# Kernel tuning notes

Hardware: AMD Instinct MI355X
Metric: run time of the kernel (lower is better)

## Reference

```python
import jax, jax.numpy as jnp
import numpy as np
from jax import lax

IMAGE_SIZE = 512
MIN_LEVEL, MAX_LEVEL = 3, 7
NUM_SCALES = 3
RATIOS = (1.0, 0.5, 2.0)
BASE_SCALE = 4
PRE_NMS = 5000
POST_NMS = 100
IOU_THR = 0.5
SCORE_THR = 0.2
NUM_CLASSES = 90
BATCH = 8


def _anchors():
    """Multiscale anchors [N,4] in (y1,x1,y2,x2) pixel coords, N=49104 for 512."""
    all_boxes = []
    for level in range(MIN_LEVEL, MAX_LEVEL + 1):
        stride = 2 ** level
        feat = IMAGE_SIZE // stride
        cy = (np.arange(feat, dtype=np.float32) + 0.5) * stride
        cx = (np.arange(feat, dtype=np.float32) + 0.5) * stride
        yv, xv = np.meshgrid(cy, cx, indexing='ij')
        yv = yv.reshape(-1)
        xv = xv.reshape(-1)
        half = []  # (half_h, half_w) per anchor config, 9 per cell
        for i in range(NUM_SCALES):
            base = (2.0 ** (i / 3.0)) * stride * BASE_SCALE
            for r in RATIOS:
                half.append((base / np.sqrt(r) / 2.0, base * np.sqrt(r) / 2.0))
        half = np.asarray(half, dtype=np.float32)  # [9,2]
        boxes = np.stack([
            yv[:, None] - half[None, :, 0],
            xv[:, None] - half[None, :, 1],
            yv[:, None] + half[None, :, 0],
            xv[:, None] + half[None, :, 1],
        ], axis=-1)  # [feat*feat, 9, 4]
        all_boxes.append(boxes.reshape(-1, 4))
    return np.concatenate(all_boxes, axis=0).astype(np.float32)


def setup_inputs() -> dict:
    key = jax.random.key(0)
    k1, k2 = jax.random.split(key)
    n = 49104
    box_deltas = jax.random.normal(k1, (BATCH, n, 4), jnp.float32) * 0.1
    cls_logits = jax.random.normal(k2, (BATCH, n, NUM_CLASSES), jnp.float32)
    return {"box_deltas": box_deltas, "cls_logits": cls_logits}


def _decode(anchors, deltas):
    # Delta2Box with mean=None/std=None: standard (dy,dx,dh,dw) decode.
    ah = anchors[:, 2] - anchors[:, 0]
    aw = anchors[:, 3] - anchors[:, 1]
    acy = (anchors[:, 0] + anchors[:, 2]) * 0.5
    acx = (anchors[:, 1] + anchors[:, 3]) * 0.5
    dy, dx, dh, dw = deltas[..., 0], deltas[..., 1], deltas[..., 2], deltas[..., 3]
    cy = dy * ah + acy
    cx = dx * aw + acx
    h = jnp.exp(dh) * ah
    w = jnp.exp(dw) * aw
    return jnp.stack([cy - h * 0.5, cx - w * 0.5, cy + h * 0.5, cx + w * 0.5], axis=-1)


def _iou_one_many(box, boxes):
    yy1 = jnp.maximum(box[0], boxes[:, 0])
    xx1 = jnp.maximum(box[1], boxes[:, 1])
    yy2 = jnp.minimum(box[2], boxes[:, 2])
    xx2 = jnp.minimum(box[3], boxes[:, 3])
    inter = jnp.maximum(yy2 - yy1, 0.0) * jnp.maximum(xx2 - xx1, 0.0)
    a1 = (box[2] - box[0]) * (box[3] - box[1])
    a2 = (boxes[:, 2] - boxes[:, 0]) * (boxes[:, 3] - boxes[:, 1])
    return inter / (a1 + a2 - inter + 1e-8)


def _nms_single(boxes, scores):
    # Greedy NMS over K boxes, at most POST_NMS selections. boxes [K,4], scores [K].
    @jax.checkpoint
    def step(s, _):
        i = jnp.argmax(s)
        sc = s[i]
        b = boxes[i]
        valid = sc > SCORE_THR
        suppress = _iou_one_many(b, boxes) > IOU_THR  # includes self
        s = jnp.where(suppress, jnp.float32(-1.0), s)
        out_b = jnp.where(valid, b, jnp.zeros_like(b))
        out_s = jnp.where(valid, sc, jnp.float32(0.0))
        return s, (out_b, out_s)
    _, (sel_b, sel_s) = lax.scan(step, scores, None, length=POST_NMS)
    return sel_b, sel_s  # [POST,4], [POST]


def reference(box_deltas, cls_logits):
    anchors = jnp.asarray(_anchors())
    boxes = _decode(anchors, box_deltas)                      # [B,N,4]
    boxes = jnp.clip(boxes / jnp.float32(IMAGE_SIZE), 0.0, 1.0)
    scores = jax.nn.sigmoid(cls_logits)                       # [B,N,C]
    scores_t = jnp.swapaxes(scores, 1, 2)                     # [B,C,N]
    top_s, top_i = lax.top_k(scores_t, PRE_NMS)               # [B,C,K]
    B = boxes.shape[0]
    bidx = jnp.arange(B)[:, None, None]
    top_b = boxes[bidx, top_i]                                # [B,C,K,4]
    sel_b, sel_s = jax.vmap(jax.vmap(_nms_single))(top_b, top_s)  # [B,C,P,4],[B,C,P]
    cls_ids = jnp.broadcast_to(
        jnp.arange(NUM_CLASSES, dtype=jnp.float32)[None, :, None], sel_s.shape)
    flat_s = sel_s.reshape(B, -1)
    flat_b = sel_b.reshape(B, -1, 4)
    flat_c = cls_ids.reshape(B, -1)
    out_s, idx = lax.top_k(flat_s, POST_NMS)                  # combine over classes
    bi = jnp.arange(B)[:, None]
    out_b = flat_b[bi, idx]
    out_c = flat_c[bi, idx]
    valid = jnp.sum((out_s > 0).astype(jnp.int32), axis=1)
    return out_b, out_s, out_c, valid
```

## Files before the change

### kernel.cpp

```cpp
#include <hip/hip_runtime.h>
#include <math.h>


#define NANCH 49104
#define NB 8
#define NC 90
#define NBC 720
#define POSTN 100
#define T1CAP 512
#define CHUNK 512
#define NCH 96
#define LCAP 32
#define EDGE 0.93f
#define PRECHK 2.0f


__device__ __forceinline__ float sigmoid_ref(float x) {
  if (x >= 0.0f) return __fdiv_rn(1.0f, __fadd_rn(1.0f, expf(-x)));
  float e = expf(x);
  return __fdiv_rn(e, __fadd_rn(1.0f, e));
}

__device__ __forceinline__ float iou_ref(float4 a, float4 b) {
  float yy1 = fmaxf(a.x, b.x);
  float xx1 = fmaxf(a.y, b.y);
  float yy2 = fminf(a.z, b.z);
  float xx2 = fminf(a.w, b.w);
  float ih = fmaxf(__fsub_rn(yy2, yy1), 0.0f);
  float iw = fmaxf(__fsub_rn(xx2, xx1), 0.0f);
  float inter = __fmul_rn(ih, iw);
  float a1 = __fmul_rn(__fsub_rn(a.z, a.x), __fsub_rn(a.w, a.y));
  float a2 = __fmul_rn(__fsub_rn(b.z, b.x), __fsub_rn(b.w, b.y));
  float den = __fadd_rn(__fsub_rn(__fadd_rn(a1, a2), inter), 1e-8f);
  return __fdiv_rn(inter, den);
}


__global__ __launch_bounds__(256) void k_anchors(float4* __restrict__ anchors,
                                                 unsigned int* __restrict__ gcnt,
                                                 unsigned int* __restrict__ oflow) {
  int n = blockIdx.x * 256 + threadIdx.x;
  if (n < NBC) { gcnt[n] = 0u; oflow[n] = 0u; }
  if (n >= NANCH) return;
  int l, off;
  if (n < 36864)      { l = 0; off = 0; }
  else if (n < 46080) { l = 1; off = 36864; }
  else if (n < 48384) { l = 2; off = 46080; }
  else if (n < 48960) { l = 3; off = 48384; }
  else                { l = 4; off = 48960; }
  int stride = 8 << l;
  int feat = 64 >> l;
  int r = n - off;
  int cell = r / 9, a = r - cell * 9;
  int iy = cell / feat, ix = cell - iy * feat;
  int isc = a / 3, ir = a - isc * 3;
  double base = exp2((double)isc / 3.0) * (double)stride * 4.0;
  double rt = (ir == 0) ? 1.0 : (ir == 1 ? 0.5 : 2.0);
  double sq = sqrt(rt);
  float hh = (float)(base / sq / 2.0);
  float hw = (float)(base * sq / 2.0);
  float cy = __fmul_rn(__fadd_rn((float)iy, 0.5f), (float)stride);
  float cx = __fmul_rn(__fadd_rn((float)ix, 0.5f), (float)stride);
  anchors[n] = make_float4(__fsub_rn(cy, hh), __fsub_rn(cx, hw),
                           __fadd_rn(cy, hh), __fadd_rn(cx, hw));
}


__global__ __launch_bounds__(256) void k_decode(const float4* __restrict__ deltas,
                                                const float4* __restrict__ anchors,
                                                float4* __restrict__ boxes) {
  int i = blockIdx.x * 256 + threadIdx.x;
  if (i >= NB * NANCH) return;
  int n = i % NANCH;
  float4 a = anchors[n];
  float4 d = deltas[i];
  float ah = __fsub_rn(a.z, a.x);
  float aw = __fsub_rn(a.w, a.y);
  float acy = __fmul_rn(__fadd_rn(a.x, a.z), 0.5f);
  float acx = __fmul_rn(__fadd_rn(a.y, a.w), 0.5f);
  float cy = __fadd_rn(__fmul_rn(d.x, ah), acy);
  float cx = __fadd_rn(__fmul_rn(d.y, aw), acx);
  float h = __fmul_rn(expf(d.z), ah);
  float w = __fmul_rn(expf(d.w), aw);
  float y1 = __fsub_rn(cy, __fmul_rn(h, 0.5f));
  float x1 = __fsub_rn(cx, __fmul_rn(w, 0.5f));
  float y2 = __fadd_rn(cy, __fmul_rn(h, 0.5f));
  float x2 = __fadd_rn(cx, __fmul_rn(w, 0.5f));
  const float inv = 0.001953125f;
  y1 = fminf(fmaxf(__fmul_rn(y1, inv), 0.0f), 1.0f);
  x1 = fminf(fmaxf(__fmul_rn(x1, inv), 0.0f), 1.0f);
  y2 = fminf(fmaxf(__fmul_rn(y2, inv), 0.0f), 1.0f);
  x2 = fminf(fmaxf(__fmul_rn(x2, inv), 0.0f), 1.0f);
  boxes[i] = make_float4(y1, x1, y2, x2);
}


__global__ __launch_bounds__(256) void k_scan(const float4* __restrict__ logits4,
                                              unsigned long long* __restrict__ gcand,
                                              unsigned int* __restrict__ gcnt,
                                              unsigned int* __restrict__ oflow) {
  int b = blockIdx.y;
  int ch = blockIdx.x;
  int n0 = ch * CHUNK;
  int rows = min(CHUNK, NANCH - n0);
  const float4* base = logits4 + ((size_t)b * NANCH + n0) * 90 / 4;
  int tot4 = rows * 90 / 4;
  int tid = threadIdx.x;

  __shared__ unsigned long long lc[NC * LCAP];
  __shared__ unsigned int lcnt[NC];
  for (int c = tid; c < NC; c += 256) lcnt[c] = 0u;
  __syncthreads();

  for (int e4 = tid; e4 < tot4; e4 += 1024) {
    float4 v[4];
#pragma unroll
    for (int k = 0; k < 4; k++) {
      int idx = e4 + k * 256;
      if (idx < tot4) v[k] = base[idx];
    }
#pragma unroll
    for (int k = 0; k < 4; k++) {
      int idx = e4 + k * 256;
      if (idx >= tot4) break;
      float xs[4] = {v[k].x, v[k].y, v[k].z, v[k].w};
#pragma unroll
      for (int j = 0; j < 4; j++) {
        float x = xs[j];
        if (x >= PRECHK) {
          float s = sigmoid_ref(x);
          if (s >= EDGE) {
            int e = idx * 4 + j;
            int r = e / 90, c = e - r * 90;
            unsigned int pos = atomicAdd(&lcnt[c], 1u);
            if (pos < LCAP) {
              int n = n0 + r;
              lc[c * LCAP + pos] =
                  ((unsigned long long)__float_as_uint(s) << 32) |
                  (unsigned int)(65535 - n);
            }
          }
        }
      }
    }
  }
  __syncthreads();

  if (tid < NC) {
    unsigned int cnt = lcnt[tid];
    int bc = b * NC + tid;
    if (cnt > LCAP) {
      atomicOr(&oflow[bc], 1u);
      cnt = LCAP;
    }
    if (cnt > 0) {
      unsigned int pos0 = atomicAdd(&gcnt[bc], cnt);
      for (unsigned int k = 0; k < cnt; k++) {
        unsigned int p = pos0 + k;
        if (p < T1CAP) gcand[(size_t)bc * T1CAP + p] = lc[tid * LCAP + k];
      }
    }
  }
}


__global__ __launch_bounds__(256) void k_nms_t1(
    const unsigned long long* __restrict__ gcand,
    const unsigned int* __restrict__ gcnt, const unsigned int* __restrict__ oflow,
    const float4* __restrict__ boxes, float* __restrict__ sel_s,
    float4* __restrict__ sel_b, int* __restrict__ flags) {
  int bc = blockIdx.x;
  int b = bc / NC;
  int tid = threadIdx.x;

  __shared__ unsigned long long cand[T1CAP];
  __shared__ float4 cbox[T1CAP];
  __shared__ unsigned char alive[T1CAP];
  __shared__ float4 s_selbox[POSTN];
  __shared__ float s_sels[POSTN];
  __shared__ int s_nsel;

  unsigned int cnt = gcnt[bc];
  bool overflow = (cnt > (unsigned)T1CAP) || (oflow[bc] != 0u);
  int M = (int)min(cnt, (unsigned)T1CAP);
  for (int e = tid; e < T1CAP; e += 256)
    cand[e] = (e < M) ? gcand[(size_t)bc * T1CAP + e] : 0ull;
  if (tid == 0) s_nsel = 0;
  __syncthreads();

  for (int k = 2; k <= T1CAP; k <<= 1) {
    for (int j = k >> 1; j > 0; j >>= 1) {
      int t = tid;
      int i = ((t & ~(j - 1)) << 1) | (t & (j - 1));
      int p = i | j;
      unsigned long long a = cand[i], bb = cand[p];
      bool up = ((i & k) == 0);
      if (up ? (a < bb) : (a > bb)) { cand[i] = bb; cand[p] = a; }
      __syncthreads();
    }
  }

  for (int e = tid; e < M; e += 256) {
    int n = 65535 - (int)(cand[e] & 0xFFFFull);
    cbox[e] = boxes[(size_t)b * NANCH + n];
    alive[e] = 1;
  }
  __syncthreads();

  for (int i = 0; i < M; i++) {
    if (s_nsel >= POSTN) break;
    if (!alive[i]) continue;
    float4 bi = cbox[i];
    float sc = __uint_as_float((unsigned int)(cand[i] >> 32));
    if (!(iou_ref(bi, bi) > 0.5f)) {
      if (tid == 0) {
        for (int p = s_nsel; p < POSTN; p++) { s_selbox[p] = bi; s_sels[p] = sc; }
        s_nsel = POSTN;
      }
      __syncthreads();
      break;
    }
    for (int t = i + 1 + tid; t < M; t += 256)
      if (alive[t] && iou_ref(cbox[t], bi) > 0.5f) alive[t] = 0;
    if (tid == 0) {
      s_selbox[s_nsel] = bi;
      s_sels[s_nsel] = sc;
      s_nsel = s_nsel + 1;
    }
    __syncthreads();
  }
  __syncthreads();
  int ns = s_nsel;

  bool bad = overflow || (ns < POSTN);
  if (tid == 0) flags[bc] = bad ? 1 : 0;
  if (bad) return;
  for (int p = tid; p < POSTN; p += 256) {
    float s0 = s_sels[p];
    bool valid = (s0 > 0.2f);
    sel_s[bc * POSTN + p] = valid ? s0 : 0.0f;
    sel_b[bc * POSTN + p] = valid ? s_selbox[p] : make_float4(0, 0, 0, 0);
  }
}


__global__ __launch_bounds__(256) void k_flagall(int* __restrict__ flags) {
  int i = blockIdx.x * 256 + threadIdx.x;
  if (i < NBC) flags[i] = 1;
}


template <int CAP, int RANK>
__global__ __launch_bounds__(256) void k_nms_fb(const float* __restrict__ logits,
                                                const float4* __restrict__ boxes,
                                                float* __restrict__ sel_s,
                                                float4* __restrict__ sel_b,
                                                const int* __restrict__ flags) {
  int bc = blockIdx.x;
  if (flags[bc] == 0) return;
  int b = bc / NC;
  int c = bc - b * NC;
  int tid = threadIdx.x;

  __shared__ unsigned int s_key[CAP];
  __shared__ unsigned short s_idx[CAP];
  __shared__ __align__(16) unsigned char s_pool[8192];
  __shared__ unsigned int s_bsum[256];
  __shared__ unsigned char s_alive[512];
  __shared__ float4 s_selbox[POSTN];
  __shared__ float s_sels[POSTN];
  __shared__ int s_cnt, s_nsel, s_cutbin;

  const float* lrow = logits + (size_t)b * NANCH * 90 + c;

  unsigned int* hist = (unsigned int*)s_pool;
  for (int e = tid; e < 2048; e += 256) hist[e] = 0u;
  if (tid == 0) { s_cnt = 0; s_nsel = 0; s_cutbin = 0; }
  __syncthreads();

  for (int n = tid; n < NANCH; n += 256) {
    float s = sigmoid_ref(lrow[(size_t)n * 90]);
    int bin = (int)(s * 2048.0f);
    if (bin > 2047) bin = 2047;
    atomicAdd(&hist[bin], 1u);
  }
  __syncthreads();
  unsigned int loc = 0;
#pragma unroll
  for (int k = 0; k < 8; k++) loc += hist[tid * 8 + k];
  s_bsum[tid] = loc;
  __syncthreads();
  if (tid == 0) {
    unsigned int cum = 0;
    int bin = 0;
    bool fnd = false;
    for (int t = 255; t >= 0 && !fnd; t--) {
      if (cum + s_bsum[t] >= (unsigned)RANK) {
        for (int kk = 7; kk >= 0; kk--) {
          unsigned int h = hist[t * 8 + kk];
          if (cum + h >= (unsigned)RANK) { bin = t * 8 + kk; fnd = true; break; }
          cum += h;
        }
      } else {
        cum += s_bsum[t];
      }
    }
    s_cutbin = bin;
  }
  __syncthreads();
  float edge = __fmul_rn((float)s_cutbin, (1.0f / 2048.0f));

  for (int n = tid; n < NANCH; n += 256) {
    float s = sigmoid_ref(lrow[(size_t)n * 90]);
    if (s >= edge) {
      int pos = atomicAdd(&s_cnt, 1);
      if (pos < CAP) {
        s_key[pos] = __float_as_uint(s);
        s_idx[pos] = (unsigned short)n;
      }
    }
  }
  __syncthreads();
  int M = s_cnt;
  if (M > CAP) M = CAP;
  for (int e = M + tid; e < CAP; e += 256) { s_key[e] = 0u; s_idx[e] = 0xFFFFu; }
  __syncthreads();

  for (int k = 2; k <= CAP; k <<= 1) {
    for (int j = k >> 1; j > 0; j >>= 1) {
      for (int t = tid; t < CAP / 2; t += 256) {
        int i = ((t & ~(j - 1)) << 1) | (t & (j - 1));
        int p = i | j;
        unsigned int ka = s_key[i], kb = s_key[p];
        unsigned short ia = s_idx[i], ib = s_idx[p];
        bool up = ((i & k) == 0);
        bool g = (ka < kb) || (ka == kb && ia > ib);
        bool l = (kb < ka) || (ka == kb && ib > ia);
        if (up ? g : l) {
          s_key[i] = kb; s_key[p] = ka;
          s_idx[i] = ib; s_idx[p] = ia;
        }
      }
      __syncthreads();
    }
  }

  float4* cbox = (float4*)s_pool;
  int L = (M < 5000) ? M : 5000;
  for (int base = 0; base < L; base += 512) {
    int cn = min(512, L - base);
    int ns0 = s_nsel;
    if (ns0 >= POSTN) break;
    for (int t = tid; t < cn; t += 256) {
      int n = s_idx[base + t];
      float4 bx = boxes[(size_t)b * NANCH + n];
      bool al = true;
      for (int s = 0; s < ns0; s++) {
        if (iou_ref(bx, s_selbox[s]) > 0.5f) { al = false; break; }
      }
      cbox[t] = bx;
      s_alive[t] = al ? 1 : 0;
    }
    __syncthreads();
    for (int i = 0; i < cn; i++) {
      if (s_nsel >= POSTN) break;
      if (!s_alive[i]) continue;
      float4 bi = cbox[i];
      float sc = __uint_as_float(s_key[base + i]);
      if (!(iou_ref(bi, bi) > 0.5f)) {
        if (tid == 0) {
          for (int p = s_nsel; p < POSTN; p++) { s_selbox[p] = bi; s_sels[p] = sc; }
          s_nsel = POSTN;
        }
        __syncthreads();
        break;
      }
      for (int t = tid; t < cn; t += 256) {
        if (t > i && s_alive[t] && iou_ref(cbox[t], bi) > 0.5f) s_alive[t] = 0;
      }
      if (tid == 0) {
        s_selbox[s_nsel] = bi;
        s_sels[s_nsel] = sc;
        s_nsel = s_nsel + 1;
      }
      __syncthreads();
    }
    __syncthreads();
    if (s_nsel >= POSTN) break;
  }
  __syncthreads();
  int ns = s_nsel;
  for (int p = tid; p < POSTN; p += 256) {
    float sc = 0.0f;
    float4 bx = make_float4(0.0f, 0.0f, 0.0f, 0.0f);
    if (p < ns) {
      float s0 = s_sels[p];
      if (s0 > 0.2f) { sc = s0; bx = s_selbox[p]; }
    }
    sel_s[bc * POSTN + p] = sc;
    sel_b[bc * POSTN + p] = bx;
  }
}


__global__ __launch_bounds__(256) void k_final(const float* __restrict__ sel_s,
                                               const float4* __restrict__ sel_b,
                                               float* __restrict__ out) {
  int b = blockIdx.x;
  int tid = threadIdx.x;
  __shared__ float key[9000];
  __shared__ int ptr[NC];
  __shared__ unsigned long long wred[4];
  __shared__ unsigned int win_k[POSTN];
  __shared__ int win_e[POSTN];
  for (int e = tid; e < 9000; e += 256) key[e] = sel_s[(size_t)b * 9000 + e];
  if (tid < NC) ptr[tid] = 0;
  __syncthreads();
  int lane = tid & 63, wid = tid >> 6;
  for (int p = 0; p < POSTN; p++) {
    unsigned long long v = 0ull;
    if (tid < NC) {
      int pp = ptr[tid];
      if (pp < POSTN) {
        int e = tid * POSTN + pp;
        v = ((unsigned long long)__float_as_uint(key[e]) << 32) |
            (unsigned int)(16383 - e);
      }
    }
    for (int d = 32; d > 0; d >>= 1) {
      unsigned long long o = __shfl_down(v, (unsigned)d, 64);
      if (o > v) v = o;
    }
    if (lane == 0) wred[wid] = v;
    __syncthreads();
    if (tid == 0) {
      unsigned long long w = wred[0];
      if (wred[1] > w) w = wred[1];
      int e = 16383 - (int)(w & 0x3FFFull);
      win_k[p] = (unsigned int)(w >> 32);
      win_e[p] = e;
      ptr[e / POSTN] = (e % POSTN) + 1;
    }
    __syncthreads();
  }
  if (tid < POSTN) {
    int p = tid;
    unsigned int k = win_k[p];
    int e = win_e[p];
    float4 bx = sel_b[(size_t)b * 9000 + e];
    ((float4*)out)[b * POSTN + p] = bx;
    out[3200 + b * POSTN + p] = __uint_as_float(k);
    out[4000 + b * POSTN + p] = (float)(e / POSTN);
  }
  if (tid == 0) {
    int v = 0;
    for (int p = 0; p < POSTN; p++) v += (win_k[p] != 0u) ? 1 : 0;
    out[4800 + b] = (float)v;
  }
}


extern "C" void kernel_launch(void* const* d_in, const int* in_sizes, int n_in,
                              void* d_out, int out_size, void* d_ws, size_t ws_size,
                              hipStream_t stream) {
  const float* deltas = (const float*)d_in[0];
  const float* logits = (const float*)d_in[1];
  float* out = (float*)d_out;
  char* ws = (char*)d_ws;

  size_t off = 0;
  auto take = [&](size_t bytes) -> char* {
    char* p = ws + off;
    off += (bytes + 255) & ~(size_t)255;
    return p;
  };
  float4* anchors = (float4*)take((size_t)NANCH * 16);
  float4* boxes = (float4*)take((size_t)NB * NANCH * 16);
  float* sel_s = (float*)take((size_t)NBC * POSTN * 4);
  float4* sel_b = (float4*)take((size_t)NBC * POSTN * 16);
  int* flags = (int*)take((size_t)NBC * 4);
  unsigned int* gcnt = (unsigned int*)take((size_t)NBC * 4);
  unsigned int* oflow = (unsigned int*)take((size_t)NBC * 4);
  unsigned long long* gcand =
      (unsigned long long*)take((size_t)NBC * T1CAP * 8);
  bool fits = (off <= ws_size);

  k_anchors<<<dim3((NANCH + 255) / 256), dim3(256), 0, stream>>>(anchors, gcnt,
                                                                 oflow);
  k_decode<<<dim3((NB * NANCH + 255) / 256), dim3(256), 0, stream>>>(
      (const float4*)deltas, anchors, boxes);
  if (fits) {
    k_scan<<<dim3(NCH, NB), dim3(256), 0, stream>>>((const float4*)logits,
                                                    gcand, gcnt, oflow);
    k_nms_t1<<<dim3(NBC), dim3(256), 0, stream>>>(gcand, gcnt, oflow, boxes,
                                                  sel_s, sel_b, flags);
  } else {
    k_flagall<<<dim3((NBC + 255) / 256), dim3(256), 0, stream>>>(flags);
  }
  k_nms_fb<8192, 5000><<<dim3(NBC), dim3(256), 0, stream>>>(logits, boxes,
                                                            sel_s, sel_b, flags);
  k_final<<<dim3(NB), dim3(256), 0, stream>>>(sel_s, sel_b, out);
}
```

Measured before the change: 341.0 us.

## Run NMS and final merge on single wavefronts with register masks and shuffles

Shrinks the per-class NMS kernel and the final cross-class merge to a single 64-lane wavefront. Alive flags move into per-thread register bitmasks, and the next surviving candidate is found with a shuffle-min, which removes per-iteration shared-memory state and block barriers. The bitonic sort length now adapts to the candidate count. The final merge keeps per-class pointers in registers and uses an xor-shuffle argmax instead of shared reductions with two barriers per step. The cost is less parallelism per block for the sort, the IoU sweep and the loads.

```diff
diff --git a/kernel.cpp b/kernel.cpp
--- a/kernel.cpp
+++ b/kernel.cpp
@@ -164,7 +164,7 @@
 }
 
 
-__global__ __launch_bounds__(256) void k_nms_t1(
+__global__ __launch_bounds__(64) void k_nms_t1(
     const unsigned long long* __restrict__ gcand,
     const unsigned int* __restrict__ gcnt, const unsigned int* __restrict__ oflow,
     const float4* __restrict__ boxes, float* __restrict__ sel_s,
@@ -175,67 +175,96 @@
 
   __shared__ unsigned long long cand[T1CAP];
   __shared__ float4 cbox[T1CAP];
-  __shared__ unsigned char alive[T1CAP];
   __shared__ float4 s_selbox[POSTN];
   __shared__ float s_sels[POSTN];
-  __shared__ int s_nsel;
 
   unsigned int cnt = gcnt[bc];
   bool overflow = (cnt > (unsigned)T1CAP) || (oflow[bc] != 0u);
   int M = (int)min(cnt, (unsigned)T1CAP);
-  for (int e = tid; e < T1CAP; e += 256)
+  for (int e = tid; e < T1CAP; e += 64)
     cand[e] = (e < M) ? gcand[(size_t)bc * T1CAP + e] : 0ull;
-  if (tid == 0) s_nsel = 0;
-  __syncthreads();
-
-  for (int k = 2; k <= T1CAP; k <<= 1) {
+  __syncthreads();
+
+  int SN = (M <= 128) ? 128 : (M <= 256) ? 256 : 512;
+  int np = SN >> 1;
+  for (int k = 2; k <= SN; k <<= 1) {
     for (int j = k >> 1; j > 0; j >>= 1) {
-      int t = tid;
-      int i = ((t & ~(j - 1)) << 1) | (t & (j - 1));
-      int p = i | j;
-      unsigned long long a = cand[i], bb = cand[p];
-      bool up = ((i & k) == 0);
-      if (up ? (a < bb) : (a > bb)) { cand[i] = bb; cand[p] = a; }
+      unsigned long long a[4], bb[4];
+      int ii[4];
+#pragma unroll
+      for (int q = 0; q < 4; q++) {
+        int t = tid + (q << 6);
+        if (t < np) {
+          int i = ((t & ~(j - 1)) << 1) | (t & (j - 1));
+          ii[q] = i;
+          a[q] = cand[i];
+          bb[q] = cand[i | j];
+        } else {
+          ii[q] = -1;
+        }
+      }
+#pragma unroll
+      for (int q = 0; q < 4; q++) {
+        if (ii[q] >= 0) {
+          bool up = ((ii[q] & k) == 0);
+          if (up ? (a[q] < bb[q]) : (a[q] > bb[q])) {
+            cand[ii[q]] = bb[q];
+            cand[ii[q] | j] = a[q];
+          }
+        }
+      }
       __syncthreads();
     }
   }
 
-  for (int e = tid; e < M; e += 256) {
-    int n = 65535 - (int)(cand[e] & 0xFFFFull);
-    cbox[e] = boxes[(size_t)b * NANCH + n];
-    alive[e] = 1;
-  }
-  __syncthreads();
-
-  for (int i = 0; i < M; i++) {
-    if (s_nsel >= POSTN) break;
-    if (!alive[i]) continue;
+  unsigned int amask = 0u;
+#pragma unroll
+  for (int q = 0; q < 8; q++) {
+    int t = tid + (q << 6);
+    if (t < M) {
+      int n = 65535 - (int)(cand[t] & 0xFFFFull);
+      cbox[t] = boxes[(size_t)b * NANCH + n];
+      amask |= (1u << q);
+    }
+  }
+  __syncthreads();
+
+  int nsel = 0;
+  int i = 0;
+  while (i < M && nsel < POSTN) {
     float4 bi = cbox[i];
     float sc = __uint_as_float((unsigned int)(cand[i] >> 32));
     if (!(iou_ref(bi, bi) > 0.5f)) {
       if (tid == 0) {
-        for (int p = s_nsel; p < POSTN; p++) { s_selbox[p] = bi; s_sels[p] = sc; }
-        s_nsel = POSTN;
-      }
-      __syncthreads();
+        for (int p = nsel; p < POSTN; p++) { s_selbox[p] = bi; s_sels[p] = sc; }
+      }
+      nsel = POSTN;
       break;
     }
-    for (int t = i + 1 + tid; t < M; t += 256)
-      if (alive[t] && iou_ref(cbox[t], bi) > 0.5f) alive[t] = 0;
-    if (tid == 0) {
-      s_selbox[s_nsel] = bi;
-      s_sels[s_nsel] = sc;
-      s_nsel = s_nsel + 1;
-    }
-    __syncthreads();
-  }
-  __syncthreads();
-  int ns = s_nsel;
-
-  bool bad = overflow || (ns < POSTN);
+    if (tid == 0) { s_selbox[nsel] = bi; s_sels[nsel] = sc; }
+    nsel++;
+    int nxt = M;
+#pragma unroll
+    for (int q = 0; q < 8; q++) {
+      int t = tid + (q << 6);
+      if (((amask >> q) & 1u) && t > i) {
+        if (iou_ref(cbox[t], bi) > 0.5f) amask &= ~(1u << q);
+        else nxt = min(nxt, t);
+      }
+    }
+#pragma unroll
+    for (int d = 1; d < 64; d <<= 1) {
+      int o = __shfl_xor(nxt, d, 64);
+      nxt = min(nxt, o);
+    }
+    i = nxt;
+  }
+  __syncthreads();
+
+  bool bad = overflow || (nsel < POSTN);
   if (tid == 0) flags[bc] = bad ? 1 : 0;
   if (bad) return;
-  for (int p = tid; p < POSTN; p += 256) {
+  for (int p = tid; p < POSTN; p += 64) {
     float s0 = s_sels[p];
     bool valid = (s0 > 0.2f);
     sel_s[bc * POSTN + p] = valid ? s0 : 0.0f;
@@ -403,48 +432,45 @@
 }
 
 
-__global__ __launch_bounds__(256) void k_final(const float* __restrict__ sel_s,
-                                               const float4* __restrict__ sel_b,
-                                               float* __restrict__ out) {
+__global__ __launch_bounds__(64) void k_final(const float* __restrict__ sel_s,
+                                              const float4* __restrict__ sel_b,
+                                              float* __restrict__ out) {
   int b = blockIdx.x;
   int tid = threadIdx.x;
   __shared__ float key[9000];
-  __shared__ int ptr[NC];
-  __shared__ unsigned long long wred[4];
   __shared__ unsigned int win_k[POSTN];
   __shared__ int win_e[POSTN];
-  for (int e = tid; e < 9000; e += 256) key[e] = sel_s[(size_t)b * 9000 + e];
-  if (tid < NC) ptr[tid] = 0;
-  __syncthreads();
-  int lane = tid & 63, wid = tid >> 6;
+  for (int e = tid; e < 9000; e += 64) key[e] = sel_s[(size_t)b * 9000 + e];
+  int p0 = 0, p1 = 0;
+  int c1 = tid + 64;
+  __syncthreads();
   for (int p = 0; p < POSTN; p++) {
     unsigned long long v = 0ull;
-    if (tid < NC) {
-      int pp = ptr[tid];
-      if (pp < POSTN) {
-        int e = tid * POSTN + pp;
-        v = ((unsigned long long)__float_as_uint(key[e]) << 32) |
-            (unsigned int)(16383 - e);
-      }
-    }
-    for (int d = 32; d > 0; d >>= 1) {
-      unsigned long long o = __shfl_down(v, (unsigned)d, 64);
+    if (p0 < POSTN) {
+      int e = tid * POSTN + p0;
+      v = ((unsigned long long)__float_as_uint(key[e]) << 32) |
+          (unsigned int)(16383 - e);
+    }
+    if (c1 < NC && p1 < POSTN) {
+      int e = c1 * POSTN + p1;
+      unsigned long long v2 = ((unsigned long long)__float_as_uint(key[e]) << 32) |
+                              (unsigned int)(16383 - e);
+      if (v2 > v) v = v2;
+    }
+#pragma unroll
+    for (int d = 1; d < 64; d <<= 1) {
+      unsigned long long o = __shfl_xor(v, d, 64);
       if (o > v) v = o;
     }
-    if (lane == 0) wred[wid] = v;
-    __syncthreads();
-    if (tid == 0) {
-      unsigned long long w = wred[0];
-      if (wred[1] > w) w = wred[1];
-      int e = 16383 - (int)(w & 0x3FFFull);
-      win_k[p] = (unsigned int)(w >> 32);
-      win_e[p] = e;
-      ptr[e / POSTN] = (e % POSTN) + 1;
-    }
-    __syncthreads();
-  }
-  if (tid < POSTN) {
-    int p = tid;
+    int e = 16383 - (int)(v & 0x3FFFull);
+    if (tid == 0) { win_k[p] = (unsigned int)(v >> 32); win_e[p] = e; }
+    int cls = e / POSTN;
+    int pp = e - cls * POSTN;
+    if (cls == tid) p0 = pp + 1;
+    else if (cls == c1) p1 = pp + 1;
+  }
+  __syncthreads();
+  for (int p = tid; p < POSTN; p += 64) {
     unsigned int k = win_k[p];
     int e = win_e[p];
     float4 bx = sel_b[(size_t)b * 9000 + e];
@@ -452,11 +478,11 @@
     out[3200 + b * POSTN + p] = __uint_as_float(k);
     out[4000 + b * POSTN + p] = (float)(e / POSTN);
   }
-  if (tid == 0) {
-    int v = 0;
-    for (int p = 0; p < POSTN; p++) v += (win_k[p] != 0u) ? 1 : 0;
-    out[4800 + b] = (float)v;
-  }
+  int vcnt = 0;
+  for (int p = tid; p < POSTN; p += 64) vcnt += (win_k[p] != 0u) ? 1 : 0;
+#pragma unroll
+  for (int d = 1; d < 64; d <<= 1) vcnt += __shfl_xor(vcnt, d, 64);
+  if (tid == 0) out[4800 + b] = (float)vcnt;
 }
 
 
@@ -492,12 +518,12 @@
   if (fits) {
     k_scan<<<dim3(NCH, NB), dim3(256), 0, stream>>>((const float4*)logits,
                                                     gcand, gcnt, oflow);
-    k_nms_t1<<<dim3(NBC), dim3(256), 0, stream>>>(gcand, gcnt, oflow, boxes,
-                                                  sel_s, sel_b, flags);
+    k_nms_t1<<<dim3(NBC), dim3(64), 0, stream>>>(gcand, gcnt, oflow, boxes,
+                                                 sel_s, sel_b, flags);
   } else {
     k_flagall<<<dim3((NBC + 255) / 256), dim3(256), 0, stream>>>(flags);
   }
   k_nms_fb<8192, 5000><<<dim3(NBC), dim3(256), 0, stream>>>(logits, boxes,
                                                             sel_s, sel_b, flags);
-  k_final<<<dim3(NB), dim3(256), 0, stream>>>(sel_s, sel_b, out);
-}
+  k_final<<<dim3(NB), dim3(64), 0, stream>>>(sel_s, sel_b, out);
+}
```

New measurement: 412.7 us. 1.21x slower.
